# Performance work log

Hardware: AMD Instinct MI355X
Metric: run time of the kernel (lower is better)

The kernel has to match this reference:

```python
import jax, jax.numpy as jnp
import numpy as np

N = 50000
E = 800000
IN_DIM = 128
OUT_DIM = 128
HEADS = 4
HEAD_DIM = OUT_DIM // HEADS  # 32


def setup_inputs() -> dict:
    key = jax.random.key(0)
    k1, k2, k3, k4 = jax.random.split(key, 4)
    x = jax.random.normal(k1, (N, IN_DIM), dtype=jnp.float32)
    edge_index = jax.random.randint(k2, (2, E), 0, N, dtype=jnp.int32)
    # nn.Linear(in_dim, out_dim): weight [out_dim, in_dim]
    W = jax.random.normal(k3, (OUT_DIM, IN_DIM), dtype=jnp.float32) * (1.0 / np.sqrt(IN_DIM))
    # nn.Linear(2*head_dim, 1): weight [1, 2*head_dim] -> flattened [2*head_dim]
    a_w = jax.random.normal(k4, (2 * HEAD_DIM,), dtype=jnp.float32) * (1.0 / np.sqrt(2 * HEAD_DIM))
    return {"x": x, "edge_index": edge_index, "W": W, "a_w": a_w}


def reference(x, edge_index, W, a_w):
    n = x.shape[0]
    Wx = (x @ W.T).reshape(n, HEADS, HEAD_DIM)          # [N,H,D]
    src, dst = edge_index[0], edge_index[1]
    Wx_src = Wx[src]                                     # [E,H,D]
    Wx_dst = Wx[dst]                                     # [E,H,D]
    # a([Wx_src || Wx_dst]) = Wx_src @ a_src + Wx_dst @ a_dst
    a_src, a_dst = a_w[:HEAD_DIM], a_w[HEAD_DIM:]
    e = jnp.einsum('ehd,d->eh', Wx_src, a_src) + jnp.einsum('ehd,d->eh', Wx_dst, a_dst)
    e = jax.nn.leaky_relu(e, negative_slope=0.2)         # [E,H]
    # numerically-stable segment softmax over incoming edges of each dst node
    e_max = jax.ops.segment_max(e, dst, num_segments=n)  # [N,H], -inf for empty
    e_exp = jnp.exp(e - e_max[dst])                      # [E,H]
    denom = jax.ops.segment_sum(e_exp, dst, num_segments=n)  # [N,H]
    alpha = e_exp / (denom[dst] + 1e-8)                  # [E,H] (dropout=0 -> identity)
    weighted = alpha[..., None] * Wx_src                 # [E,H,D]
    out = jax.ops.segment_sum(weighted, dst, num_segments=n)  # [N,H,D]
    return jax.nn.elu(out.reshape(n, OUT_DIM))
```

## Files before the change

kernel.cpp:

```cpp
#include <hip/hip_runtime.h>
#include <hip/hip_bf16.h>
#include <math.h>

#define HEADS 4
#define NBKT 196
#define CAPB 4608
#define CAPP 6656

typedef short bf16x8 __attribute__((ext_vector_type(8)));
typedef float f32x4 __attribute__((ext_vector_type(4)));
typedef unsigned short ushort8 __attribute__((ext_vector_type(8)));

__device__ __forceinline__ float lrelu(float v) { return v >= 0.f ? v : 0.2f * v; }

__device__ __forceinline__ unsigned short f2bf(float f) {
    unsigned u = __float_as_uint(f);
    return (unsigned short)((u + 0x7FFF + ((u >> 16) & 1)) >> 16);
}

__device__ __forceinline__ unsigned pk2bf(float a, float b) {
    __hip_bfloat162 h = __float22bfloat162_rn(make_float2(a, b));
    unsigned u;
    __builtin_memcpy(&u, &h, 4);
    return u;
}

__global__ __launch_bounds__(256, 2) void fused_kernel(const float* __restrict__ x,
                                                       const float* __restrict__ W,
                                                       const float* __restrict__ aw,
                                                       const int* __restrict__ ei,
                                                       unsigned short* __restrict__ Wxh,
                                                       float* __restrict__ s_src,
                                                       float* __restrict__ s_dst,
                                                       int* __restrict__ gcur,
                                                       unsigned* __restrict__ gbuf,
                                                       int n, int E, int ngemm) {
    __shared__ __align__(16) char smem[66304];
    const int t = threadIdx.x;

    if ((int)blockIdx.x < ngemm) {
        unsigned short* Alds = (unsigned short*)smem;
        unsigned short* Blds = (unsigned short*)(smem + 32768);
        float* sawm = (float*)(smem + 65536);
        const int w = t >> 6, l = t & 63;
        const int q = l >> 4, l16 = l & 15;
        const int node0 = blockIdx.x * 128;

        if (t < 64) sawm[t] = aw[t];

#pragma unroll
        for (int i = 0; i < 8; ++i) {
            int c = i * 256 + t;
            int nl = c >> 4, k8 = c & 15;
            int gn = node0 + nl;
            if (gn >= n) gn = n - 1;
            const float4* gp = (const float4*)(x + (size_t)gn * 128 + k8 * 8);
            float4 v0 = gp[0], v1 = gp[1];
            uint4 u = make_uint4(pk2bf(v0.x, v0.y), pk2bf(v0.z, v0.w),
                                 pk2bf(v1.x, v1.y), pk2bf(v1.z, v1.w));
            int ch = (((nl >> 4) * 4 + (k8 >> 2)) * 4 + (k8 & 3)) * 16 + (nl & 15);
            *(uint4*)(&Alds[ch * 8]) = u;
        }
#pragma unroll
        for (int i = 0; i < 8; ++i) {
            int c = i * 256 + t;
            int dl = c >> 4, k8 = c & 15;
            const float4* gp = (const float4*)(W + (size_t)dl * 128 + k8 * 8);
            float4 v0 = gp[0], v1 = gp[1];
            uint4 u = make_uint4(pk2bf(v0.x, v0.y), pk2bf(v0.z, v0.w),
                                 pk2bf(v1.x, v1.y), pk2bf(v1.z, v1.w));
            int ch = (((dl >> 4) * 4 + (k8 >> 2)) * 4 + (k8 & 3)) * 16 + (dl & 15);
            *(uint4*)(&Blds[ch * 8]) = u;
        }
        __syncthreads();

        f32x4 acc[2][8];
#pragma unroll
        for (int rt = 0; rt < 2; ++rt)
#pragma unroll
            for (int ct = 0; ct < 8; ++ct) acc[rt][ct] = (f32x4){0.f, 0.f, 0.f, 0.f};

#pragma unroll
        for (int kk = 0; kk < 4; ++kk) {
            bf16x8 a0 = *(const bf16x8*)(&Alds[(((w * 2 + 0) * 4 + kk) * 64 + l) * 8]);
            bf16x8 a1 = *(const bf16x8*)(&Alds[(((w * 2 + 1) * 4 + kk) * 64 + l) * 8]);
#pragma unroll
            for (int ct = 0; ct < 8; ++ct) {
                bf16x8 b = *(const bf16x8*)(&Blds[((ct * 4 + kk) * 64 + l) * 8]);
                acc[0][ct] = __builtin_amdgcn_mfma_f32_16x16x32_bf16(a0, b, acc[0][ct], 0, 0, 0);
                acc[1][ct] = __builtin_amdgcn_mfma_f32_16x16x32_bf16(a1, b, acc[1][ct], 0, 0, 0);
            }
        }

        __syncthreads();
#pragma unroll
        for (int rt = 0; rt < 2; ++rt) {
            int nl = w * 32 + rt * 16 + q * 4;
#pragma unroll
            for (int ct = 0; ct < 8; ++ct) {
                int dim = ct * 16 + l16;
                Alds[(nl + 0) * 128 + dim] = f2bf(acc[rt][ct][0]);
                Alds[(nl + 1) * 128 + dim] = f2bf(acc[rt][ct][1]);
                Alds[(nl + 2) * 128 + dim] = f2bf(acc[rt][ct][2]);
                Alds[(nl + 3) * 128 + dim] = f2bf(acc[rt][ct][3]);
            }
        }
        __syncthreads();

#pragma unroll
        for (int i = 0; i < 8; ++i) {
            int c = i * 256 + t;
            int nl = c >> 4, d8 = c & 15;
            int gn = node0 + nl;
            ushort8 u = *(const ushort8*)(&Alds[nl * 128 + d8 * 8]);
            if (gn < n) *(ushort8*)(Wxh + (size_t)gn * 128 + d8 * 8) = u;
            float sp = 0.f, dp = 0.f;
            int ab = (d8 & 3) * 8;
#pragma unroll
            for (int j = 0; j < 8; ++j) {
                float v = __uint_as_float(((unsigned)(unsigned short)u[j]) << 16);
                sp += v * sawm[ab + j];
                dp += v * sawm[32 + ab + j];
            }
            sp += __shfl_xor(sp, 1, 64); dp += __shfl_xor(dp, 1, 64);
            sp += __shfl_xor(sp, 2, 64); dp += __shfl_xor(dp, 2, 64);
            if ((l & 3) == 0 && gn < n) {
                int h = (l & 15) >> 2;
                s_src[(size_t)gn * 4 + h] = sp;
                s_dst[(size_t)gn * 4 + h] = dp;
            }
        }
    } else {
        int* hist = (int*)smem;
        int* scanws = (int*)(smem + 1024);
        int* lbase = (int*)(smem + 2048);
        int* lcur = (int*)(smem + 3072);
        int* gb = (int*)(smem + 4096);
        unsigned* sorted = (unsigned*)(smem + 5120);
        unsigned char* bkt = (unsigned char*)(smem + 21504);

        const int blk = blockIdx.x - ngemm;
        const int b0 = blk * 4096;
        const int total = min(4096, E - b0);

        hist[t] = 0;
        __syncthreads();

        unsigned pk[16];
#pragma unroll
        for (int i = 0; i < 16; ++i) {
            int idx = i * 256 + t;
            if (idx < total) {
                int e = b0 + idx;
                unsigned s = (unsigned)ei[e], d = (unsigned)ei[E + e];
                pk[i] = s | (d << 16);
                atomicAdd(&hist[d >> 8], 1);
            }
        }
        __syncthreads();
        int v = hist[t];
        scanws[t] = v;
        __syncthreads();
        for (int off = 1; off < 256; off <<= 1) {
            int y = (t >= off) ? scanws[t - off] : 0;
            __syncthreads();
            scanws[t] += y;
            __syncthreads();
        }
        int ex = scanws[t] - v;
        lbase[t] = ex;
        lcur[t] = ex;
        if (t < NBKT) gb[t] = (v > 0) ? atomicAdd(&gcur[t], v) : 0;
        __syncthreads();
#pragma unroll
        for (int i = 0; i < 16; ++i) {
            int idx = i * 256 + t;
            if (idx < total) {
                int b = pk[i] >> 24;
                int qpos = atomicAdd(&lcur[b], 1);
                sorted[qpos] = pk[i];
                bkt[qpos] = (unsigned char)b;
            }
        }
        __syncthreads();
#pragma unroll
        for (int i = 0; i < 16; ++i) {
            int s = i * 256 + t;
            if (s < total) {
                int b = bkt[s];
                int pos = gb[b] + (s - lbase[b]);
                if (pos < CAPB) gbuf[(size_t)b * CAPB + pos] = sorted[s];
            }
        }
    }
}

__global__ __launch_bounds__(1024) void pass2_kernel(const int* __restrict__ gcur,
                                                     const unsigned* __restrict__ gbuf,
                                                     unsigned short* __restrict__ csr,
                                                     int2* __restrict__ node_info,
                                                     float* __restrict__ s_src, int n) {
    __shared__ int hist[256], scanws[256], cur[256];
    const int t = threadIdx.x;
    const int bucket = blockIdx.x;
    int cnt = gcur[bucket];
    if (cnt > CAPB) cnt = CAPB;
    const unsigned* gp = gbuf + (size_t)bucket * CAPB;

    if (bucket == 0 && t < 4) s_src[(size_t)n * 4 + t] = -1e30f;

    if (t < 256) hist[t] = 0;
    __syncthreads();

    unsigned e[5];
#pragma unroll
    for (int i = 0; i < 5; ++i) {
        int idx = i * 1024 + t;
        if (idx < cnt) {
            e[i] = gp[idx];
            atomicAdd(&hist[(e[i] >> 16) & 255], 1);
        }
    }
    __syncthreads();
    int v = 0, vp = 0;
    if (t < 256) {
        v = hist[t];
        vp = (v + 7) & ~7;
        scanws[t] = vp;
    }
    __syncthreads();
    for (int off = 1; off < 256; off <<= 1) {
        int y = 0;
        if (t < 256 && t >= off) y = scanws[t - off];
        __syncthreads();
        if (t < 256) scanws[t] += y;
        __syncthreads();
    }
    if (t < 256) {
        int ex = scanws[t] - vp;
        cur[t] = ex;
        int node = bucket * 256 + t;
        if (node < n) node_info[node] = make_int2(bucket * CAPP + ex, vp);
        for (int j = v; j < vp; ++j) csr[(size_t)bucket * CAPP + ex + j] = (unsigned short)n;
    }
    __syncthreads();
#pragma unroll
    for (int i = 0; i < 5; ++i) {
        int idx = i * 1024 + t;
        if (idx < cnt) {
            int ld = (e[i] >> 16) & 255;
            int qpos = atomicAdd(&cur[ld], 1);
            csr[(size_t)bucket * CAPP + qpos] = (unsigned short)(e[i] & 0xFFFF);
        }
    }
}

__global__ __launch_bounds__(256) void accum_kernel(const int2* __restrict__ node_info,
                                                    const unsigned short* __restrict__ csr,
                                                    const float* __restrict__ s_src,
                                                    const float* __restrict__ s_dst,
                                                    const unsigned short* __restrict__ Wxh,
                                                    float* __restrict__ out, int n) {
    int wid = threadIdx.x >> 6, lane = threadIdx.x & 63;
    int node = blockIdx.x * 4 + wid;
    if (node >= n) return;
    int l = lane & 15, grp = lane >> 4;
    int h = l >> 2;
    int2 info = node_info[node];
    int start = info.x, npairs = info.y >> 1;
    float sdn = s_dst[(size_t)node * 4 + h];
    const unsigned ONE2 = 0x3F803F80u;

    float acc[8] = {0.f, 0.f, 0.f, 0.f, 0.f, 0.f, 0.f, 0.f};
    float dsum = 0.f;
    int p = grp;
    for (; p + 4 < npairs; p += 8) {
        unsigned c0 = *(const unsigned*)(csr + start + 2 * p);
        unsigned c1 = *(const unsigned*)(csr + start + 2 * (p + 4));
        int sa0 = c0 & 0xFFFF, sa1 = c0 >> 16;
        int sb0 = c1 & 0xFFFF, sb1 = c1 >> 16;
        uint4 Ua0 = *(const uint4*)(Wxh + ((size_t)sa0 << 7) + l * 8);
        uint4 Ua1 = *(const uint4*)(Wxh + ((size_t)sa1 << 7) + l * 8);
        uint4 Ub0 = *(const uint4*)(Wxh + ((size_t)sb0 << 7) + l * 8);
        uint4 Ub1 = *(const uint4*)(Wxh + ((size_t)sb1 << 7) + l * 8);
        float wa0 = __expf(lrelu(s_src[sa0 * 4 + h] + sdn));
        float wa1 = __expf(lrelu(s_src[sa1 * 4 + h] + sdn));
        float wb0 = __expf(lrelu(s_src[sb0 * 4 + h] + sdn));
        float wb1 = __expf(lrelu(s_src[sb1 * 4 + h] + sdn));
        unsigned wpa = pk2bf(wa0, wa1);
        unsigned wpb = pk2bf(wb0, wb1);
        asm("v_dot2_f32_bf16 %0, %1, %2, %0" : "+v"(dsum) : "v"(wpa), "v"(ONE2));
        asm("v_dot2_f32_bf16 %0, %1, %2, %0" : "+v"(dsum) : "v"(wpb), "v"(ONE2));
        unsigned a0[4] = {Ua0.x, Ua0.y, Ua0.z, Ua0.w};
        unsigned a1[4] = {Ua1.x, Ua1.y, Ua1.z, Ua1.w};
        unsigned b0[4] = {Ub0.x, Ub0.y, Ub0.z, Ub0.w};
        unsigned b1[4] = {Ub1.x, Ub1.y, Ub1.z, Ub1.w};
#pragma unroll
        for (int j = 0; j < 4; ++j) {
            unsigned lo_a = __builtin_amdgcn_perm(a0[j], a1[j], 0x01000504u);
            unsigned hi_a = __builtin_amdgcn_perm(a0[j], a1[j], 0x03020706u);
            unsigned lo_b = __builtin_amdgcn_perm(b0[j], b1[j], 0x01000504u);
            unsigned hi_b = __builtin_amdgcn_perm(b0[j], b1[j], 0x03020706u);
            asm("v_dot2_f32_bf16 %0, %1, %2, %0" : "+v"(acc[2 * j]) : "v"(wpa), "v"(lo_a));
            asm("v_dot2_f32_bf16 %0, %1, %2, %0" : "+v"(acc[2 * j + 1]) : "v"(wpa), "v"(hi_a));
            asm("v_dot2_f32_bf16 %0, %1, %2, %0" : "+v"(acc[2 * j]) : "v"(wpb), "v"(lo_b));
            asm("v_dot2_f32_bf16 %0, %1, %2, %0" : "+v"(acc[2 * j + 1]) : "v"(wpb), "v"(hi_b));
        }
    }
    if (p < npairs) {
        unsigned c0 = *(const unsigned*)(csr + start + 2 * p);
        int sa0 = c0 & 0xFFFF, sa1 = c0 >> 16;
        uint4 Ua0 = *(const uint4*)(Wxh + ((size_t)sa0 << 7) + l * 8);
        uint4 Ua1 = *(const uint4*)(Wxh + ((size_t)sa1 << 7) + l * 8);
        float wa0 = __expf(lrelu(s_src[sa0 * 4 + h] + sdn));
        float wa1 = __expf(lrelu(s_src[sa1 * 4 + h] + sdn));
        unsigned wpa = pk2bf(wa0, wa1);
        asm("v_dot2_f32_bf16 %0, %1, %2, %0" : "+v"(dsum) : "v"(wpa), "v"(ONE2));
        unsigned a0[4] = {Ua0.x, Ua0.y, Ua0.z, Ua0.w};
        unsigned a1[4] = {Ua1.x, Ua1.y, Ua1.z, Ua1.w};
#pragma unroll
        for (int j = 0; j < 4; ++j) {
            unsigned lo_a = __builtin_amdgcn_perm(a0[j], a1[j], 0x01000504u);
            unsigned hi_a = __builtin_amdgcn_perm(a0[j], a1[j], 0x03020706u);
            asm("v_dot2_f32_bf16 %0, %1, %2, %0" : "+v"(acc[2 * j]) : "v"(wpa), "v"(lo_a));
            asm("v_dot2_f32_bf16 %0, %1, %2, %0" : "+v"(acc[2 * j + 1]) : "v"(wpa), "v"(hi_a));
        }
    }
#pragma unroll
    for (int m = 16; m <= 32; m <<= 1) {
#pragma unroll
        for (int j = 0; j < 8; ++j) acc[j] += __shfl_xor(acc[j], m, 64);
        dsum += __shfl_xor(dsum, m, 64);
    }
    if (grp == 0) {
        float inv = 1.f / (dsum + 1e-8f);
        float o[8];
#pragma unroll
        for (int j = 0; j < 8; ++j) {
            float v = acc[j] * inv;
            o[j] = v > 0.f ? v : (__expf(v) - 1.f);
        }
        float4* dp = (float4*)(out + (size_t)node * 128 + l * 8);
        dp[0] = make_float4(o[0], o[1], o[2], o[3]);
        dp[1] = make_float4(o[4], o[5], o[6], o[7]);
    }
}

extern "C" void kernel_launch(void* const* d_in, const int* in_sizes, int n_in,
                              void* d_out, int out_size, void* d_ws, size_t ws_size,
                              hipStream_t stream) {
    const float* x = (const float*)d_in[0];
    const int* ei = (const int*)d_in[1];
    const float* W = (const float*)d_in[2];
    const float* aw = (const float*)d_in[3];
    float* out = (float*)d_out;
    const int n = in_sizes[0] / 128;
    const int E = in_sizes[1] / 2;

    char* ws = (char*)d_ws;
    size_t off = 0;
    unsigned short* Wxh = (unsigned short*)(ws + off); off += (size_t)(n + 8) * 128 * 2;
    float* s_src = (float*)(ws + off);     off += (size_t)(n + 1) * HEADS * 4;
    float* s_dst = (float*)(ws + off);     off += (size_t)n * HEADS * 4;
    int* gcur = (int*)(ws + off);          off += 1024;
    unsigned* gbuf = (unsigned*)(ws + off); off += (size_t)NBKT * CAPB * 4;
    unsigned short* csr = (unsigned short*)(ws + off); off += (size_t)NBKT * CAPP * 2;
    int2* node_info = (int2*)(ws + off);   off += (size_t)n * 8;

    const int ngemm = (n + 127) / 128;
    const int npass1 = (E + 4095) / 4096;

    hipMemsetAsync(gcur, 0, 1024, stream);
    fused_kernel<<<ngemm + npass1, 256, 0, stream>>>(x, W, aw, ei, Wxh, s_src, s_dst,
                                                     gcur, gbuf, n, E, ngemm);
    pass2_kernel<<<npass1, 1024, 0, stream>>>(gcur, gbuf, csr, node_info, s_src, n);
    accum_kernel<<<(n + 3) / 4, 256, 0, stream>>>(node_info, csr, s_src, s_dst, Wxh, out, n);
}
```

Measured before the change: 137.3 us.

## Fuse CSR build and attention accumulation into one per-quarter-bucket kernel

Merges the pass2 CSR construction and the accumulate kernel into a single kernel. Each block takes a quarter of a 256-node bucket, builds the 64-node CSR in LDS and then aggregates from it directly. This removes a kernel launch, the global CSR and node_info round trip, and the 1024-thread block scans. In exchange, each bucket's gbuf is read four times with filtering, and there are only 784 blocks of 256 threads, so latency hiding in the gather phase may drop. Padding-sentinel init moves into the GEMM kernel and the Wxh padding row is zeroed.

Result: slower. 140.9 us (+2.6%).

```diff
diff --git a/kernel.cpp b/kernel.cpp
--- a/kernel.cpp
+++ b/kernel.cpp
@@ -5,7 +5,7 @@
 #define HEADS 4
 #define NBKT 196
 #define CAPB 4608
-#define CAPP 6656
+#define CAPQ 1792
 
 typedef short bf16x8 __attribute__((ext_vector_type(8)));
 typedef float f32x4 __attribute__((ext_vector_type(4)));
@@ -47,6 +47,10 @@
         const int node0 = blockIdx.x * 128;
 
         if (t < 64) sawm[t] = aw[t];
+        if (blockIdx.x == 0) {
+            if (t < 4) s_src[(size_t)n * 4 + t] = -1e30f;
+            if (t < 64) ((unsigned*)(Wxh + (size_t)n * 128))[t] = 0u;
+        }
 
 #pragma unroll
         for (int i = 0; i < 8; ++i) {
@@ -195,154 +199,154 @@
     }
 }
 
-__global__ __launch_bounds__(1024) void pass2_kernel(const int* __restrict__ gcur,
-                                                     const unsigned* __restrict__ gbuf,
-                                                     unsigned short* __restrict__ csr,
-                                                     int2* __restrict__ node_info,
-                                                     float* __restrict__ s_src, int n) {
-    __shared__ int hist[256], scanws[256], cur[256];
+__global__ __launch_bounds__(256) void pass2_accum(const int* __restrict__ gcur,
+                                                   const unsigned* __restrict__ gbuf,
+                                                   const float* __restrict__ s_src,
+                                                   const float* __restrict__ s_dst,
+                                                   const unsigned short* __restrict__ Wxh,
+                                                   float* __restrict__ out, int n) {
+    __shared__ int hist[64], basew[64], cur[64];
+    __shared__ __align__(16) unsigned short csrl[CAPQ];
     const int t = threadIdx.x;
-    const int bucket = blockIdx.x;
+    const int bucket = blockIdx.x >> 2;
+    const unsigned quarter = blockIdx.x & 3;
     int cnt = gcur[bucket];
     if (cnt > CAPB) cnt = CAPB;
     const unsigned* gp = gbuf + (size_t)bucket * CAPB;
 
-    if (bucket == 0 && t < 4) s_src[(size_t)n * 4 + t] = -1e30f;
-
-    if (t < 256) hist[t] = 0;
+    if (t < 64) hist[t] = 0;
     __syncthreads();
 
-    unsigned e[5];
-#pragma unroll
-    for (int i = 0; i < 5; ++i) {
-        int idx = i * 1024 + t;
+    unsigned pk[18];
+#pragma unroll
+    for (int i = 0; i < 18; ++i) {
+        int idx = i * 256 + t;
+        pk[i] = 0xFFFFFFFFu;
         if (idx < cnt) {
-            e[i] = gp[idx];
-            atomicAdd(&hist[(e[i] >> 16) & 255], 1);
+            unsigned u = gp[idx];
+            if (((u >> 22) & 3u) == quarter) {
+                pk[i] = u;
+                atomicAdd(&hist[(u >> 16) & 63], 1);
+            }
         }
     }
     __syncthreads();
-    int v = 0, vp = 0;
-    if (t < 256) {
-        v = hist[t];
-        vp = (v + 7) & ~7;
-        scanws[t] = vp;
+
+    if (t < 64) {
+        int v = hist[t];
+        int vp = (v + 7) & ~7;
+        int sc = vp;
+#pragma unroll
+        for (int off = 1; off < 64; off <<= 1) {
+            int y = __shfl_up(sc, off, 64);
+            if (t >= off) sc += y;
+        }
+        int base = sc - vp;
+        basew[t] = base;
+        cur[t] = base;
+        for (int j = v; j < vp; ++j) {
+            int pos = base + j;
+            if (pos < CAPQ) csrl[pos] = (unsigned short)n;
+        }
+        hist[t] = vp;
     }
     __syncthreads();
-    for (int off = 1; off < 256; off <<= 1) {
-        int y = 0;
-        if (t < 256 && t >= off) y = scanws[t - off];
-        __syncthreads();
-        if (t < 256) scanws[t] += y;
-        __syncthreads();
-    }
-    if (t < 256) {
-        int ex = scanws[t] - vp;
-        cur[t] = ex;
-        int node = bucket * 256 + t;
-        if (node < n) node_info[node] = make_int2(bucket * CAPP + ex, vp);
-        for (int j = v; j < vp; ++j) csr[(size_t)bucket * CAPP + ex + j] = (unsigned short)n;
+
+#pragma unroll
+    for (int i = 0; i < 18; ++i) {
+        unsigned u = pk[i];
+        if (u != 0xFFFFFFFFu) {
+            int bin = (u >> 16) & 63;
+            int pos = atomicAdd(&cur[bin], 1);
+            if (pos < CAPQ) csrl[pos] = (unsigned short)(u & 0xFFFF);
+        }
     }
     __syncthreads();
-#pragma unroll
-    for (int i = 0; i < 5; ++i) {
-        int idx = i * 1024 + t;
-        if (idx < cnt) {
-            int ld = (e[i] >> 16) & 255;
-            int qpos = atomicAdd(&cur[ld], 1);
-            csr[(size_t)bucket * CAPP + qpos] = (unsigned short)(e[i] & 0xFFFF);
-        }
-    }
-}
-
-__global__ __launch_bounds__(256) void accum_kernel(const int2* __restrict__ node_info,
-                                                    const unsigned short* __restrict__ csr,
-                                                    const float* __restrict__ s_src,
-                                                    const float* __restrict__ s_dst,
-                                                    const unsigned short* __restrict__ Wxh,
-                                                    float* __restrict__ out, int n) {
-    int wid = threadIdx.x >> 6, lane = threadIdx.x & 63;
-    int node = blockIdx.x * 4 + wid;
-    if (node >= n) return;
-    int l = lane & 15, grp = lane >> 4;
-    int h = l >> 2;
-    int2 info = node_info[node];
-    int start = info.x, npairs = info.y >> 1;
-    float sdn = s_dst[(size_t)node * 4 + h];
+
+    const int wid = t >> 6, lane = t & 63;
+    const int l = lane & 15, grp = lane >> 4, h = l >> 2;
     const unsigned ONE2 = 0x3F803F80u;
 
-    float acc[8] = {0.f, 0.f, 0.f, 0.f, 0.f, 0.f, 0.f, 0.f};
-    float dsum = 0.f;
-    int p = grp;
-    for (; p + 4 < npairs; p += 8) {
-        unsigned c0 = *(const unsigned*)(csr + start + 2 * p);
-        unsigned c1 = *(const unsigned*)(csr + start + 2 * (p + 4));
-        int sa0 = c0 & 0xFFFF, sa1 = c0 >> 16;
-        int sb0 = c1 & 0xFFFF, sb1 = c1 >> 16;
-        uint4 Ua0 = *(const uint4*)(Wxh + ((size_t)sa0 << 7) + l * 8);
-        uint4 Ua1 = *(const uint4*)(Wxh + ((size_t)sa1 << 7) + l * 8);
-        uint4 Ub0 = *(const uint4*)(Wxh + ((size_t)sb0 << 7) + l * 8);
-        uint4 Ub1 = *(const uint4*)(Wxh + ((size_t)sb1 << 7) + l * 8);
-        float wa0 = __expf(lrelu(s_src[sa0 * 4 + h] + sdn));
-        float wa1 = __expf(lrelu(s_src[sa1 * 4 + h] + sdn));
-        float wb0 = __expf(lrelu(s_src[sb0 * 4 + h] + sdn));
-        float wb1 = __expf(lrelu(s_src[sb1 * 4 + h] + sdn));
-        unsigned wpa = pk2bf(wa0, wa1);
-        unsigned wpb = pk2bf(wb0, wb1);
-        asm("v_dot2_f32_bf16 %0, %1, %2, %0" : "+v"(dsum) : "v"(wpa), "v"(ONE2));
-        asm("v_dot2_f32_bf16 %0, %1, %2, %0" : "+v"(dsum) : "v"(wpb), "v"(ONE2));
-        unsigned a0[4] = {Ua0.x, Ua0.y, Ua0.z, Ua0.w};
-        unsigned a1[4] = {Ua1.x, Ua1.y, Ua1.z, Ua1.w};
-        unsigned b0[4] = {Ub0.x, Ub0.y, Ub0.z, Ub0.w};
-        unsigned b1[4] = {Ub1.x, Ub1.y, Ub1.z, Ub1.w};
-#pragma unroll
-        for (int j = 0; j < 4; ++j) {
-            unsigned lo_a = __builtin_amdgcn_perm(a0[j], a1[j], 0x01000504u);
-            unsigned hi_a = __builtin_amdgcn_perm(a0[j], a1[j], 0x03020706u);
-            unsigned lo_b = __builtin_amdgcn_perm(b0[j], b1[j], 0x01000504u);
-            unsigned hi_b = __builtin_amdgcn_perm(b0[j], b1[j], 0x03020706u);
-            asm("v_dot2_f32_bf16 %0, %1, %2, %0" : "+v"(acc[2 * j]) : "v"(wpa), "v"(lo_a));
-            asm("v_dot2_f32_bf16 %0, %1, %2, %0" : "+v"(acc[2 * j + 1]) : "v"(wpa), "v"(hi_a));
-            asm("v_dot2_f32_bf16 %0, %1, %2, %0" : "+v"(acc[2 * j]) : "v"(wpb), "v"(lo_b));
-            asm("v_dot2_f32_bf16 %0, %1, %2, %0" : "+v"(acc[2 * j + 1]) : "v"(wpb), "v"(hi_b));
-        }
-    }
-    if (p < npairs) {
-        unsigned c0 = *(const unsigned*)(csr + start + 2 * p);
-        int sa0 = c0 & 0xFFFF, sa1 = c0 >> 16;
-        uint4 Ua0 = *(const uint4*)(Wxh + ((size_t)sa0 << 7) + l * 8);
-        uint4 Ua1 = *(const uint4*)(Wxh + ((size_t)sa1 << 7) + l * 8);
-        float wa0 = __expf(lrelu(s_src[sa0 * 4 + h] + sdn));
-        float wa1 = __expf(lrelu(s_src[sa1 * 4 + h] + sdn));
-        unsigned wpa = pk2bf(wa0, wa1);
-        asm("v_dot2_f32_bf16 %0, %1, %2, %0" : "+v"(dsum) : "v"(wpa), "v"(ONE2));
-        unsigned a0[4] = {Ua0.x, Ua0.y, Ua0.z, Ua0.w};
-        unsigned a1[4] = {Ua1.x, Ua1.y, Ua1.z, Ua1.w};
-#pragma unroll
-        for (int j = 0; j < 4; ++j) {
-            unsigned lo_a = __builtin_amdgcn_perm(a0[j], a1[j], 0x01000504u);
-            unsigned hi_a = __builtin_amdgcn_perm(a0[j], a1[j], 0x03020706u);
-            asm("v_dot2_f32_bf16 %0, %1, %2, %0" : "+v"(acc[2 * j]) : "v"(wpa), "v"(lo_a));
-            asm("v_dot2_f32_bf16 %0, %1, %2, %0" : "+v"(acc[2 * j + 1]) : "v"(wpa), "v"(hi_a));
-        }
-    }
-#pragma unroll
-    for (int m = 16; m <= 32; m <<= 1) {
-#pragma unroll
-        for (int j = 0; j < 8; ++j) acc[j] += __shfl_xor(acc[j], m, 64);
-        dsum += __shfl_xor(dsum, m, 64);
-    }
-    if (grp == 0) {
-        float inv = 1.f / (dsum + 1e-8f);
-        float o[8];
-#pragma unroll
-        for (int j = 0; j < 8; ++j) {
-            float v = acc[j] * inv;
-            o[j] = v > 0.f ? v : (__expf(v) - 1.f);
-        }
-        float4* dp = (float4*)(out + (size_t)node * 128 + l * 8);
-        dp[0] = make_float4(o[0], o[1], o[2], o[3]);
-        dp[1] = make_float4(o[4], o[5], o[6], o[7]);
+    for (int ln = wid; ln < 64; ln += 4) {
+        int node = bucket * 256 + (int)quarter * 64 + ln;
+        if (node >= n) break;
+        int start = basew[ln];
+        int npairs = hist[ln] >> 1;
+        float sdn = s_dst[(size_t)node * 4 + h];
+
+        float acc[8] = {0.f, 0.f, 0.f, 0.f, 0.f, 0.f, 0.f, 0.f};
+        float dsum = 0.f;
+        int p = grp;
+        for (; p + 4 < npairs; p += 8) {
+            unsigned c0 = *(const unsigned*)(&csrl[start + 2 * p]);
+            unsigned c1 = *(const unsigned*)(&csrl[start + 2 * (p + 4)]);
+            int sa0 = c0 & 0xFFFF, sa1 = c0 >> 16;
+            int sb0 = c1 & 0xFFFF, sb1 = c1 >> 16;
+            uint4 Ua0 = *(const uint4*)(Wxh + ((size_t)sa0 << 7) + l * 8);
+            uint4 Ua1 = *(const uint4*)(Wxh + ((size_t)sa1 << 7) + l * 8);
+            uint4 Ub0 = *(const uint4*)(Wxh + ((size_t)sb0 << 7) + l * 8);
+            uint4 Ub1 = *(const uint4*)(Wxh + ((size_t)sb1 << 7) + l * 8);
+            float wa0 = __expf(lrelu(s_src[sa0 * 4 + h] + sdn));
+            float wa1 = __expf(lrelu(s_src[sa1 * 4 + h] + sdn));
+            float wb0 = __expf(lrelu(s_src[sb0 * 4 + h] + sdn));
+            float wb1 = __expf(lrelu(s_src[sb1 * 4 + h] + sdn));
+            unsigned wpa = pk2bf(wa0, wa1);
+            unsigned wpb = pk2bf(wb0, wb1);
+            asm("v_dot2_f32_bf16 %0, %1, %2, %0" : "+v"(dsum) : "v"(wpa), "v"(ONE2));
+            asm("v_dot2_f32_bf16 %0, %1, %2, %0" : "+v"(dsum) : "v"(wpb), "v"(ONE2));
+            unsigned a0[4] = {Ua0.x, Ua0.y, Ua0.z, Ua0.w};
+            unsigned a1[4] = {Ua1.x, Ua1.y, Ua1.z, Ua1.w};
+            unsigned b0[4] = {Ub0.x, Ub0.y, Ub0.z, Ub0.w};
+            unsigned b1[4] = {Ub1.x, Ub1.y, Ub1.z, Ub1.w};
+#pragma unroll
+            for (int j = 0; j < 4; ++j) {
+                unsigned lo_a = __builtin_amdgcn_perm(a0[j], a1[j], 0x01000504u);
+                unsigned hi_a = __builtin_amdgcn_perm(a0[j], a1[j], 0x03020706u);
+                unsigned lo_b = __builtin_amdgcn_perm(b0[j], b1[j], 0x01000504u);
+                unsigned hi_b = __builtin_amdgcn_perm(b0[j], b1[j], 0x03020706u);
+                asm("v_dot2_f32_bf16 %0, %1, %2, %0" : "+v"(acc[2 * j]) : "v"(wpa), "v"(lo_a));
+                asm("v_dot2_f32_bf16 %0, %1, %2, %0" : "+v"(acc[2 * j + 1]) : "v"(wpa), "v"(hi_a));
+                asm("v_dot2_f32_bf16 %0, %1, %2, %0" : "+v"(acc[2 * j]) : "v"(wpb), "v"(lo_b));
+                asm("v_dot2_f32_bf16 %0, %1, %2, %0" : "+v"(acc[2 * j + 1]) : "v"(wpb), "v"(hi_b));
+            }
+        }
+        if (p < npairs) {
+            unsigned c0 = *(const unsigned*)(&csrl[start + 2 * p]);
+            int sa0 = c0 & 0xFFFF, sa1 = c0 >> 16;
+            uint4 Ua0 = *(const uint4*)(Wxh + ((size_t)sa0 << 7) + l * 8);
+            uint4 Ua1 = *(const uint4*)(Wxh + ((size_t)sa1 << 7) + l * 8);
+            float wa0 = __expf(lrelu(s_src[sa0 * 4 + h] + sdn));
+            float wa1 = __expf(lrelu(s_src[sa1 * 4 + h] + sdn));
+            unsigned wpa = pk2bf(wa0, wa1);
+            asm("v_dot2_f32_bf16 %0, %1, %2, %0" : "+v"(dsum) : "v"(wpa), "v"(ONE2));
+            unsigned a0[4] = {Ua0.x, Ua0.y, Ua0.z, Ua0.w};
+            unsigned a1[4] = {Ua1.x, Ua1.y, Ua1.z, Ua1.w};
+#pragma unroll
+            for (int j = 0; j < 4; ++j) {
+                unsigned lo_a = __builtin_amdgcn_perm(a0[j], a1[j], 0x01000504u);
+                unsigned hi_a = __builtin_amdgcn_perm(a0[j], a1[j], 0x03020706u);
+                asm("v_dot2_f32_bf16 %0, %1, %2, %0" : "+v"(acc[2 * j]) : "v"(wpa), "v"(lo_a));
+                asm("v_dot2_f32_bf16 %0, %1, %2, %0" : "+v"(acc[2 * j + 1]) : "v"(wpa), "v"(hi_a));
+            }
+        }
+#pragma unroll
+        for (int m = 16; m <= 32; m <<= 1) {
+#pragma unroll
+            for (int j = 0; j < 8; ++j) acc[j] += __shfl_xor(acc[j], m, 64);
+            dsum += __shfl_xor(dsum, m, 64);
+        }
+        if (grp == 0) {
+            float inv = 1.f / (dsum + 1e-8f);
+            float o[8];
+#pragma unroll
+            for (int j = 0; j < 8; ++j) {
+                float v = acc[j] * inv;
+                o[j] = v > 0.f ? v : (__expf(v) - 1.f);
+            }
+            float4* dp = (float4*)(out + (size_t)node * 128 + l * 8);
+            dp[0] = make_float4(o[0], o[1], o[2], o[3]);
+            dp[1] = make_float4(o[4], o[5], o[6], o[7]);
+        }
     }
 }
 
@@ -364,8 +368,6 @@
     float* s_dst = (float*)(ws + off);     off += (size_t)n * HEADS * 4;
     int* gcur = (int*)(ws + off);          off += 1024;
     unsigned* gbuf = (unsigned*)(ws + off); off += (size_t)NBKT * CAPB * 4;
-    unsigned short* csr = (unsigned short*)(ws + off); off += (size_t)NBKT * CAPP * 2;
-    int2* node_info = (int2*)(ws + off);   off += (size_t)n * 8;
 
     const int ngemm = (n + 127) / 128;
     const int npass1 = (E + 4095) / 4096;
@@ -373,6 +375,5 @@
     hipMemsetAsync(gcur, 0, 1024, stream);
     fused_kernel<<<ngemm + npass1, 256, 0, stream>>>(x, W, aw, ei, Wxh, s_src, s_dst,
                                                      gcur, gbuf, n, E, ngemm);
-    pass2_kernel<<<npass1, 1024, 0, stream>>>(gcur, gbuf, csr, node_info, s_src, n);
-    accum_kernel<<<(n + 3) / 4, 256, 0, stream>>>(node_info, csr, s_src, s_dst, Wxh, out, n);
-}
+    pass2_accum<<<NBKT * 4, 256, 0, stream>>>(gcur, gbuf, s_src, s_dst, Wxh, out, n);
+}
```
